# Kernel optimization log

Measured on AMD Instinct MI355X. Metric: run time of the kernel, lower is better.

The kernel has to match this reference:

```python
import jax, jax.numpy as jnp
import numpy as np

N, D, FF, NH = 500000, 128, 256, 4
GRIDS = [0.5, 1.0, 2.0]


def setup_inputs() -> dict:
    key = jax.random.key(0)
    ks = jax.random.split(key, 8)
    h = jax.random.normal(ks[0], (N, D), jnp.float32)
    coords = jax.random.uniform(ks[1], (N, 3), jnp.float32) * 8.0
    c = np.asarray(coords)
    invs, Ms = [], []
    for g in GRIDS:
        vox = np.floor(c / g).astype(np.int64)
        _, inv = np.unique(vox, axis=0, return_inverse=True)
        invs.append(jnp.asarray(inv.reshape(-1).astype(np.int32)))
        Ms.append(int(inv.max()) + 1)
    S = len(GRIDS)
    sc = 0.02
    def rn(k, shape):
        return jax.random.normal(k, shape, jnp.float32) * sc
    params = dict(
        Wqkv=rn(ks[2], (S, 3 * D, D)), bqkv=jnp.zeros((S, 3 * D), jnp.float32),
        Wo=rn(ks[3], (S, D, D)), bo=jnp.zeros((S, D), jnp.float32),
        ln1_s=jnp.ones((S, D), jnp.float32), ln1_b=jnp.zeros((S, D), jnp.float32),
        W1=rn(ks[4], (S, FF, D)), b1=jnp.zeros((S, FF), jnp.float32),
        W2=rn(ks[5], (S, D, FF)), b2=jnp.zeros((S, D), jnp.float32),
        ln2_s=jnp.ones((S, D), jnp.float32), ln2_b=jnp.zeros((S, D), jnp.float32),
        Wf=rn(ks[6], (D, D * (S + 1))), bf=jnp.zeros((D,), jnp.float32),
    )
    return dict(h=h, coords=coords, inv0=invs[0], inv1=invs[1], inv2=invs[2],
                M0=Ms[0], M1=Ms[1], M2=Ms[2], **params)


def _ln(x, s, b):
    m = x.mean(-1, keepdims=True)
    v = ((x - m) ** 2).mean(-1, keepdims=True)
    return (x - m) * jax.lax.rsqrt(v + 1e-5) * s + b


def _forward(h, invs, Ms, Wqkv, bqkv, Wo, bo, ln1_s, ln1_b, W1, b1, W2, b2, ln2_s, ln2_b, Wf, bf):
    dh = D // NH
    feats = [h]
    for i, (inv, M) in enumerate(zip(invs, Ms)):
        # scatter-mean pooling into M voxels (counts clamped >= 1)
        macro = jax.ops.segment_sum(h, inv, num_segments=M)  # [M, D]
        counts = jax.ops.segment_sum(jnp.ones((h.shape[0], 1), h.dtype), inv, num_segments=M)
        macro = macro / jnp.maximum(counts, 1.0)
        # TransformerEncoderLayer (post-norm, relu), batch of 1 -> drop batch dim
        qkv = macro @ Wqkv[i].T + bqkv[i]
        q, k, v = (t.reshape(M, NH, dh) for t in jnp.split(qkv, 3, axis=-1))
        scores = jnp.einsum('mhd,nhd->hmn', q, k) / jnp.sqrt(jnp.float32(dh))
        attn = jax.nn.softmax(scores, axis=-1)
        o = jnp.einsum('hmn,nhd->mhd', attn, v).reshape(M, D) @ Wo[i].T + bo[i]
        x = _ln(macro + o, ln1_s[i], ln1_b[i])
        ffo = jax.nn.relu(x @ W1[i].T + b1[i]) @ W2[i].T + b2[i]
        x = _ln(x + ffo, ln2_s[i], ln2_b[i])
        feats.append(x[inv])  # broadcast gather back to particles [N, D]
    return jnp.concatenate(feats, axis=-1) @ Wf.T + bf


def reference(h, coords, inv0, inv1, inv2, M0, M1, M2, Wqkv, bqkv, Wo, bo, ln1_s, ln1_b, W1, b1, W2, b2, ln2_s, ln2_b, Wf, bf):
    return _forward(h, (inv0, inv1, inv2), (M0, M1, M2), Wqkv, bqkv, Wo, bo,
                    ln1_s, ln1_b, W1, b1, W2, b2, ln2_s, ln2_b, Wf, bf)
```

## Files before the change

kernel.cpp:

```cpp
#include <hip/hip_runtime.h>
#include <hip/hip_bf16.h>

#define MC 4096
#define DD 128
#define NHH 4
#define DH 32
#define FFD 256
#define NS 3
#define NSPLIT 4
#define PLEN 1024

typedef __attribute__((ext_vector_type(8))) short short8_t;
typedef __attribute__((ext_vector_type(4))) float f32x4;

__device__ __forceinline__ int getM(int s, const int* M0, const int* M1, const int* M2) {
    return (s == 0) ? *M0 : (s == 1) ? *M1 : *M2;
}

__device__ __forceinline__ unsigned short f2bf(float f) {
    unsigned int u = __float_as_uint(f);
    u += 0x7FFFu + ((u >> 16) & 1u);
    return (unsigned short)(u >> 16);
}

__device__ __forceinline__ short8_t pack8(float4 a, float4 b) {
    short8_t r;
    r[0] = (short)f2bf(a.x); r[1] = (short)f2bf(a.y);
    r[2] = (short)f2bf(a.z); r[3] = (short)f2bf(a.w);
    r[4] = (short)f2bf(b.x); r[5] = (short)f2bf(b.y);
    r[6] = (short)f2bf(b.z); r[7] = (short)f2bf(b.w);
    return r;
}

__device__ __forceinline__ f32x4 max4(f32x4 a, f32x4 b) {
    f32x4 r;
    r[0] = fmaxf(a[0], b[0]); r[1] = fmaxf(a[1], b[1]);
    r[2] = fmaxf(a[2], b[2]); r[3] = fmaxf(a[3], b[3]);
    return r;
}
__device__ __forceinline__ f32x4 shflx4(f32x4 a, int m) {
    f32x4 r;
    r[0] = __shfl_xor(a[0], m); r[1] = __shfl_xor(a[1], m);
    r[2] = __shfl_xor(a[2], m); r[3] = __shfl_xor(a[3], m);
    return r;
}
__device__ __forceinline__ f32x4 exp4(f32x4 a) {
    f32x4 r;
    r[0] = __expf(a[0]); r[1] = __expf(a[1]);
    r[2] = __expf(a[2]); r[3] = __expf(a[3]);
    return r;
}

__global__ void k_parent(const int* __restrict__ inv0, const int* __restrict__ inv1,
                         const int* __restrict__ inv2,
                         int* __restrict__ parent10, int* __restrict__ parent21,
                         int* __restrict__ cnt, int N)
{
    int n = blockIdx.x * blockDim.x + threadIdx.x;
    if (n >= N) return;
    int i0 = inv0[n];
    parent10[i0] = inv1[n];
    parent21[inv1[n]] = inv2[n];
    atomicAdd(&cnt[i0], 1);
}

__global__ void k_scan(const int* __restrict__ cnt, int* __restrict__ offs)
{
    __shared__ int arr[1024];
    int tid = threadIdx.x;
    int base = tid * 4;
    int c0 = cnt[base], c1 = cnt[base + 1], c2 = cnt[base + 2], c3 = cnt[base + 3];
    int tot = c0 + c1 + c2 + c3;
    arr[tid] = tot;
    __syncthreads();
    for (int off = 1; off < 1024; off <<= 1) {
        int v = (tid >= off) ? arr[tid - off] : 0;
        __syncthreads();
        arr[tid] += v;
        __syncthreads();
    }
    int excl = arr[tid] - tot;
    offs[base] = excl;
    offs[base + 1] = excl + c0;
    offs[base + 2] = excl + c0 + c1;
    offs[base + 3] = excl + c0 + c1 + c2;
}

__global__ void k_place(const int* __restrict__ inv0, const int* __restrict__ offs,
                        int* __restrict__ fill, int* __restrict__ order, int N)
{
    int n = blockIdx.x * blockDim.x + threadIdx.x;
    if (n >= N) return;
    int i0 = inv0[n];
    int pos = offs[i0] + atomicAdd(&fill[i0], 1);
    order[pos] = n;
}

__global__ __launch_bounds__(256) void k_pool(const float* __restrict__ h,
                                              const int* __restrict__ order,
                                              const int* __restrict__ offs,
                                              const int* __restrict__ cnt,
                                              float* __restrict__ sum0, float* __restrict__ cnt0,
                                              const int* __restrict__ M0)
{
    int v = blockIdx.x;
    if (v >= *M0) return;
    int beg = offs[v], len = cnt[v];
    int tid = threadIdx.x;
    int dg = tid & 31;
    int rs = tid >> 5;
    const int* op = order + beg;

    float ax = 0.f, ay = 0.f, az = 0.f, aw = 0.f;
    int j = rs;
    for (; j + 8 < len; j += 16) {
        int r0 = op[j];
        int r1 = op[j + 8];
        float4 a = *(const float4*)(h + (size_t)r0 * DD + dg * 4);
        float4 b = *(const float4*)(h + (size_t)r1 * DD + dg * 4);
        ax += a.x + b.x; ay += a.y + b.y; az += a.z + b.z; aw += a.w + b.w;
    }
    if (j < len) {
        int r0 = op[j];
        float4 a = *(const float4*)(h + (size_t)r0 * DD + dg * 4);
        ax += a.x; ay += a.y; az += a.z; aw += a.w;
    }

    __shared__ __align__(16) float red[8][DD];
    *(float4*)&red[rs][dg * 4] = make_float4(ax, ay, az, aw);
    __syncthreads();
    if (tid < 32) {
        float4 t0 = *(const float4*)&red[0][tid * 4];
        float4 t1 = *(const float4*)&red[1][tid * 4];
        float4 t2 = *(const float4*)&red[2][tid * 4];
        float4 t3 = *(const float4*)&red[3][tid * 4];
        float4 t4 = *(const float4*)&red[4][tid * 4];
        float4 t5 = *(const float4*)&red[5][tid * 4];
        float4 t6 = *(const float4*)&red[6][tid * 4];
        float4 t7 = *(const float4*)&red[7][tid * 4];
        float4 r;
        r.x = ((t0.x + t1.x) + (t2.x + t3.x)) + ((t4.x + t5.x) + (t6.x + t7.x));
        r.y = ((t0.y + t1.y) + (t2.y + t3.y)) + ((t4.y + t5.y) + (t6.y + t7.y));
        r.z = ((t0.z + t1.z) + (t2.z + t3.z)) + ((t4.z + t5.z) + (t6.z + t7.z));
        r.w = ((t0.w + t1.w) + (t2.w + t3.w)) + ((t4.w + t5.w) + (t6.w + t7.w));
        *(float4*)(sum0 + (size_t)v * DD + tid * 4) = r;
        if (tid == 0) cnt0[v] = (float)len;
    }
}

__global__ void k_rollup(const float* __restrict__ sumSrc, const float* __restrict__ cntSrc,
                         const int* __restrict__ parent,
                         float* __restrict__ sumDst, float* __restrict__ cntDst,
                         const int* __restrict__ Msrc, int cap)
{
    int idx = blockIdx.x * blockDim.x + threadIdx.x;
    int v = idx >> 7, d = idx & 127;
    int Ms = *Msrc;
    if (Ms > cap) Ms = cap;
    if (v >= Ms) return;
    int p = parent[v];
    atomicAdd(&sumDst[(size_t)p * DD + d], sumSrc[idx]);
    if (d == 0) atomicAdd(&cntDst[p], cntSrc[v]);
}

__global__ void k_finalize(float* __restrict__ macro, const float* __restrict__ counts,
                           const int* M0, const int* M1, const int* M2)
{
    int idx = blockIdx.x * blockDim.x + threadIdx.x;
    int s = idx / (MC * DD);
    int r = (idx >> 7) & (MC - 1);
    if (r >= getM(s, M0, M1, M2)) return;
    float c = counts[s * MC + r];
    macro[idx] /= fmaxf(c, 1.0f);
}

__global__ void k_b0frag(const float* __restrict__ Wf, unsigned short* __restrict__ b0f)
{
    int idx = blockIdx.x * 256 + threadIdx.x;
    int j = idx & 7, l = (idx >> 3) & 63, kt = (idx >> 9) & 3, nt = idx >> 11;
    int d = nt * 16 + (l & 15);
    int k = kt * 32 + (l >> 4) * 8 + j;
    b0f[idx] = f2bf(Wf[(size_t)d * (4 * DD) + k]);
}

__global__ void k_qkv(const float* __restrict__ macro, const float* __restrict__ Wqkv,
                      const float* __restrict__ bqkv, float* __restrict__ qkv,
                      const int* M0, const int* M1, const int* M2)
{
    int s = blockIdx.y;
    int Ms = getM(s, M0, M1, M2);
    int row0 = blockIdx.x * 8;
    if (row0 >= Ms) return;
    __shared__ __align__(16) float mac[8][DD];
    int tid = threadIdx.x;
    for (int e = tid; e < 8 * DD; e += 256) {
        int r = e >> 7, d = e & 127;
        int row = row0 + r;
        mac[r][d] = (row < Ms) ? macro[(size_t)s * MC * DD + (size_t)row * DD + d] : 0.0f;
    }
    __syncthreads();
    for (int j = tid; j < 3 * DD; j += 256) {
        const float* w = Wqkv + ((size_t)s * 3 * DD + j) * DD;
        float b = bqkv[s * 3 * DD + j];
        float acc[8];
#pragma unroll
        for (int r = 0; r < 8; ++r) acc[r] = b;
        for (int k = 0; k < DD; k += 4) {
            float4 w4 = *(const float4*)(w + k);
#pragma unroll
            for (int r = 0; r < 8; ++r) {
                float4 m4 = *(const float4*)&mac[r][k];
                acc[r] += w4.x * m4.x + w4.y * m4.y + w4.z * m4.z + w4.w * m4.w;
            }
        }
        for (int r = 0; r < 8; ++r) {
            int row = row0 + r;
            if (row < Ms) qkv[((size_t)s * MC + row) * (3 * DD) + j] = acc[r];
        }
    }
}

__global__ __launch_bounds__(256) void k_attn_part(const float* __restrict__ qkv,
                                                   float* __restrict__ part_o,
                                                   float* __restrict__ part_ml,
                                                   const int* M0, const int* M1, const int* M2)
{
    int z = blockIdx.z;
    int s = z / NSPLIT, part = z % NSPLIT;
    int head = blockIdx.y;
    int Ms = getM(s, M0, M1, M2);
    int q0 = blockIdx.x * 64;
    if (q0 >= Ms) return;
    int kstart = part * PLEN;
    if (kstart >= Ms) return;
    int kend = kstart + PLEN; if (kend > Ms) kend = Ms;

    __shared__ __align__(16) unsigned short kf[2][4][64][8];
    __shared__ __align__(16) unsigned short vf[2][2][2][64][8];
    __shared__ __align__(16) unsigned short pf[4][16][80];

    int tid = threadIdx.x;
    int wave = tid >> 6, lane = tid & 63;
    int c = lane & 15, g = lane >> 4;

    const float* base = qkv + (size_t)s * MC * 3 * DD;
    const float* Qb = base + head * DH;
    const float* Kb = base + DD + head * DH;
    const float* Vb = base + 2 * DD + head * DH;

    short8_t qfrag = {0,0,0,0,0,0,0,0};
    {
        int qr = q0 + wave * 16 + c;
        if (qr < Ms) {
            const float* qp = Qb + (size_t)qr * 3 * DD + g * 8;
            qfrag = pack8(*(const float4*)qp, *(const float4*)(qp + 4));
        }
    }

    f32x4 o0 = {0.f, 0.f, 0.f, 0.f}, o1 = {0.f, 0.f, 0.f, 0.f};
    f32x4 mreg = {-1e30f, -1e30f, -1e30f, -1e30f};
    f32x4 lreg = {0.f, 0.f, 0.f, 0.f};
    const float scale = 0.1767766952966369f;

    int sko = tid >> 2, sg = tid & 3;
    int s_nt = sko >> 4;
    int s_l  = (sko & 15) | (sg << 4);
    int s_ks = sko >> 5, s_kk = sko & 31;
    int s_j  = s_kk & 7, s_hi = (s_kk >> 3) & 3;
    int s_vnt = sg >> 1, s_db = (sg & 1) * 8;

    auto STAGE = [&](int buf, int kb) {
        {
            int key = kb + sko;
            short8_t kv = {0,0,0,0,0,0,0,0};
            if (key < kend) {
                const float* kr = Kb + (size_t)key * 3 * DD + sg * 8;
                kv = pack8(*(const float4*)kr, *(const float4*)(kr + 4));
            }
            *(short8_t*)&kf[buf][s_nt][s_l][0] = kv;
        }
        {
            int key = kb + sko;
            float4 a = make_float4(0.f, 0.f, 0.f, 0.f);
            float4 b = make_float4(0.f, 0.f, 0.f, 0.f);
            if (key < kend) {
                const float* vr = Vb + (size_t)key * 3 * DD + sg * 8;
                a = *(const float4*)vr;
                b = *(const float4*)(vr + 4);
            }
            unsigned short* vslot = &vf[buf][s_ks][s_vnt][0][0];
            vslot[((s_db + 0) | (s_hi << 4)) * 8 + s_j] = f2bf(a.x);
            vslot[((s_db + 1) | (s_hi << 4)) * 8 + s_j] = f2bf(a.y);
            vslot[((s_db + 2) | (s_hi << 4)) * 8 + s_j] = f2bf(a.z);
            vslot[((s_db + 3) | (s_hi << 4)) * 8 + s_j] = f2bf(a.w);
            vslot[((s_db + 4) | (s_hi << 4)) * 8 + s_j] = f2bf(b.x);
            vslot[((s_db + 5) | (s_hi << 4)) * 8 + s_j] = f2bf(b.y);
            vslot[((s_db + 6) | (s_hi << 4)) * 8 + s_j] = f2bf(b.z);
            vslot[((s_db + 7) | (s_hi << 4)) * 8 + s_j] = f2bf(b.w);
        }
    };

    STAGE(0, kstart);
    __syncthreads();
    int cur = 0;

    for (int kb = kstart; kb < kend; kb += 64) {
        if (kb + 64 < kend) STAGE(cur ^ 1, kb + 64);

        f32x4 zero = {0.f, 0.f, 0.f, 0.f};
        short8_t kf0 = *(const short8_t*)&kf[cur][0][lane][0];
        short8_t kf1 = *(const short8_t*)&kf[cur][1][lane][0];
        short8_t kf2 = *(const short8_t*)&kf[cur][2][lane][0];
        short8_t kf3 = *(const short8_t*)&kf[cur][3][lane][0];
        f32x4 a0 = __builtin_amdgcn_mfma_f32_16x16x32_bf16(qfrag, kf0, zero, 0, 0, 0);
        f32x4 a1 = __builtin_amdgcn_mfma_f32_16x16x32_bf16(qfrag, kf1, zero, 0, 0, 0);
        f32x4 a2 = __builtin_amdgcn_mfma_f32_16x16x32_bf16(qfrag, kf2, zero, 0, 0, 0);
        f32x4 a3 = __builtin_amdgcn_mfma_f32_16x16x32_bf16(qfrag, kf3, zero, 0, 0, 0);

        f32x4 neg = {-1e30f, -1e30f, -1e30f, -1e30f};
        a0 = (kb +  0 + c < kend) ? a0 * scale : neg;
        a1 = (kb + 16 + c < kend) ? a1 * scale : neg;
        a2 = (kb + 32 + c < kend) ? a2 * scale : neg;
        a3 = (kb + 48 + c < kend) ? a3 * scale : neg;

        f32x4 rmax = max4(max4(a0, a1), max4(a2, a3));
        rmax = max4(rmax, shflx4(rmax, 1));
        rmax = max4(rmax, shflx4(rmax, 2));
        rmax = max4(rmax, shflx4(rmax, 4));
        rmax = max4(rmax, shflx4(rmax, 8));
        f32x4 mnew = max4(mreg, rmax);
        f32x4 alpha = exp4(mreg - mnew);
        mreg = mnew;
        lreg = lreg * alpha;
        o0 = o0 * alpha;
        o1 = o1 * alpha;

        a0 = exp4(a0 - mnew);
        a1 = exp4(a1 - mnew);
        a2 = exp4(a2 - mnew);
        a3 = exp4(a3 - mnew);
        f32x4 rsum = (a0 + a1) + (a2 + a3);
        rsum = rsum + shflx4(rsum, 1);
        rsum = rsum + shflx4(rsum, 2);
        rsum = rsum + shflx4(rsum, 4);
        rsum = rsum + shflx4(rsum, 8);
        lreg = lreg + rsum;

        {
            unsigned short* prow = &pf[wave][0][0];
            int rb = g * 4;
            prow[(rb + 0) * 80 +  0 + c] = f2bf(a0[0]);
            prow[(rb + 1) * 80 +  0 + c] = f2bf(a0[1]);
            prow[(rb + 2) * 80 +  0 + c] = f2bf(a0[2]);
            prow[(rb + 3) * 80 +  0 + c] = f2bf(a0[3]);
            prow[(rb + 0) * 80 + 16 + c] = f2bf(a1[0]);
            prow[(rb + 1) * 80 + 16 + c] = f2bf(a1[1]);
            prow[(rb + 2) * 80 + 16 + c] = f2bf(a1[2]);
            prow[(rb + 3) * 80 + 16 + c] = f2bf(a1[3]);
            prow[(rb + 0) * 80 + 32 + c] = f2bf(a2[0]);
            prow[(rb + 1) * 80 + 32 + c] = f2bf(a2[1]);
            prow[(rb + 2) * 80 + 32 + c] = f2bf(a2[2]);
            prow[(rb + 3) * 80 + 32 + c] = f2bf(a2[3]);
            prow[(rb + 0) * 80 + 48 + c] = f2bf(a3[0]);
            prow[(rb + 1) * 80 + 48 + c] = f2bf(a3[1]);
            prow[(rb + 2) * 80 + 48 + c] = f2bf(a3[2]);
            prow[(rb + 3) * 80 + 48 + c] = f2bf(a3[3]);
        }

        {
            short8_t p0 = *(const short8_t*)&pf[wave][c][ 0 + g * 8];
            short8_t v00 = *(const short8_t*)&vf[cur][0][0][lane][0];
            short8_t v01 = *(const short8_t*)&vf[cur][0][1][lane][0];
            o0 = __builtin_amdgcn_mfma_f32_16x16x32_bf16(p0, v00, o0, 0, 0, 0);
            o1 = __builtin_amdgcn_mfma_f32_16x16x32_bf16(p0, v01, o1, 0, 0, 0);
            short8_t p1 = *(const short8_t*)&pf[wave][c][32 + g * 8];
            short8_t v10 = *(const short8_t*)&vf[cur][1][0][lane][0];
            short8_t v11 = *(const short8_t*)&vf[cur][1][1][lane][0];
            o0 = __builtin_amdgcn_mfma_f32_16x16x32_bf16(p1, v10, o0, 0, 0, 0);
            o1 = __builtin_amdgcn_mfma_f32_16x16x32_bf16(p1, v11, o1, 0, 0, 0);
        }

        __syncthreads();
        cur ^= 1;
    }

    int rec = ((s * NHH + head) * 64 + blockIdx.x) * NSPLIT + part;
    float* po = part_o + (size_t)rec * 2048;
    int qb = wave * 16 + g * 4;
    po[(qb + 0) * 32 + c] = o0[0];
    po[(qb + 1) * 32 + c] = o0[1];
    po[(qb + 2) * 32 + c] = o0[2];
    po[(qb + 3) * 32 + c] = o0[3];
    po[(qb + 0) * 32 + 16 + c] = o1[0];
    po[(qb + 1) * 32 + 16 + c] = o1[1];
    po[(qb + 2) * 32 + 16 + c] = o1[2];
    po[(qb + 3) * 32 + 16 + c] = o1[3];
    if (c == 0) {
        part_ml[rec * 128 + qb + 0] = mreg[0];
        part_ml[rec * 128 + qb + 1] = mreg[1];
        part_ml[rec * 128 + qb + 2] = mreg[2];
        part_ml[rec * 128 + qb + 3] = mreg[3];
        part_ml[rec * 128 + 64 + qb + 0] = lreg[0];
        part_ml[rec * 128 + 64 + qb + 1] = lreg[1];
        part_ml[rec * 128 + 64 + qb + 2] = lreg[2];
        part_ml[rec * 128 + 64 + qb + 3] = lreg[3];
    }
}

__global__ void k_attn_comb(const float* __restrict__ part_o, const float* __restrict__ part_ml,
                            float* __restrict__ attno,
                            const int* M0, const int* M1, const int* M2)
{
    int s = blockIdx.z, head = blockIdx.y;
    int Ms = getM(s, M0, M1, M2);
    int q0 = blockIdx.x * 64;
    if (q0 >= Ms) return;
    int tid = threadIdx.x;
    int qi = tid >> 2, sub = tid & 3;
    int nparts = (Ms + PLEN - 1) / PLEN;
    if (nparts > NSPLIT) nparts = NSPLIT;
    int recbase = ((s * NHH + head) * 64 + blockIdx.x) * NSPLIT;

    float m = -1e30f;
    for (int p = 0; p < nparts; ++p)
        m = fmaxf(m, part_ml[(recbase + p) * 128 + qi]);
    float L = 0.f;
    float4 A0 = {0,0,0,0}, A1 = {0,0,0,0};
    for (int p = 0; p < nparts; ++p) {
        float mp = part_ml[(recbase + p) * 128 + qi];
        float lp = part_ml[(recbase + p) * 128 + 64 + qi];
        float w = __expf(mp - m);
        L += lp * w;
        const float* po = part_o + (size_t)(recbase + p) * 2048;
        float4 a = *(const float4*)(po + qi * 32 + sub * 4);
        float4 b = *(const float4*)(po + qi * 32 + (sub + 4) * 4);
        A0.x += a.x * w; A0.y += a.y * w; A0.z += a.z * w; A0.w += a.w * w;
        A1.x += b.x * w; A1.y += b.y * w; A1.z += b.z * w; A1.w += b.w * w;
    }
    if (q0 + qi < Ms) {
        float inv = 1.0f / fmaxf(L, 1e-30f);
        size_t orow = ((size_t)s * MC + q0 + qi) * DD + head * DH;
        float4 r0 = make_float4(A0.x * inv, A0.y * inv, A0.z * inv, A0.w * inv);
        float4 r1 = make_float4(A1.x * inv, A1.y * inv, A1.z * inv, A1.w * inv);
        *(float4*)(attno + orow + sub * 4) = r0;
        *(float4*)(attno + orow + (sub + 4) * 4) = r1;
    }
}

__global__ __launch_bounds__(256) void k_layer(const float* __restrict__ macro,
                                               const float* __restrict__ attno,
                                               const float* __restrict__ Wo, const float* __restrict__ bo,
                                               const float* __restrict__ ln1s, const float* __restrict__ ln1b,
                                               const float* __restrict__ W1, const float* __restrict__ b1,
                                               const float* __restrict__ W2, const float* __restrict__ b2,
                                               const float* __restrict__ ln2s, const float* __restrict__ ln2b,
                                               const float* __restrict__ Wf,
                                               float* __restrict__ y,
                                               const int* M0, const int* M1, const int* M2)
{
    int s = blockIdx.y;
    int Ms = getM(s, M0, M1, M2);
    int row0 = blockIdx.x * 8;
    if (row0 >= Ms) return;
    __shared__ __align__(16) float os8[8][DD];
    __shared__ __align__(16) float xr8[8][DD];
    __shared__ __align__(16) float ts8[8][FFD];
    __shared__ float mv[8][2];
    int tid = threadIdx.x;
    int rr = tid >> 5, tt = tid & 31;

    {
        int row = row0 + rr;
        float4 v = make_float4(0.f, 0.f, 0.f, 0.f);
        if (row < Ms) v = *(const float4*)(attno + ((size_t)s * MC + row) * DD + tt * 4);
        *(float4*)&os8[rr][tt * 4] = v;
    }
    __syncthreads();

    float acc[8];

    if (tid < DD) {
        const float* w = Wo + ((size_t)s * DD + tid) * DD;
        float b = bo[s * DD + tid];
#pragma unroll
        for (int r = 0; r < 8; ++r) acc[r] = b;
        for (int k = 0; k < DD; k += 4) {
            float4 w4 = *(const float4*)(w + k);
#pragma unroll
            for (int r = 0; r < 8; ++r) {
                float4 m4 = *(const float4*)&os8[r][k];
                acc[r] += w4.x * m4.x + w4.y * m4.y + w4.z * m4.z + w4.w * m4.w;
            }
        }
#pragma unroll
        for (int r = 0; r < 8; ++r) {
            int row = row0 + r;
            float res = (row < Ms) ? macro[((size_t)s * MC + row) * DD + tid] : 0.f;
            xr8[r][tid] = acc[r] + res;
        }
    }
    __syncthreads();

    {
        float4 v = *(const float4*)&xr8[rr][tt * 4];
        float su = v.x + v.y + v.z + v.w;
        float sq = v.x * v.x + v.y * v.y + v.z * v.z + v.w * v.w;
        for (int off = 16; off >= 1; off >>= 1) { su += __shfl_xor(su, off); sq += __shfl_xor(sq, off); }
        if (tt == 0) { mv[rr][0] = su; mv[rr][1] = sq; }
    }
    __syncthreads();
    {
        float mean = mv[rr][0] * (1.0f / DD);
        float var = fmaxf(mv[rr][1] * (1.0f / DD) - mean * mean, 0.0f);
        float rstd = rsqrtf(var + 1e-5f);
        float4 v = *(const float4*)&xr8[rr][tt * 4];
        float4 gs = *(const float4*)(ln1s + s * DD + tt * 4);
        float4 gb = *(const float4*)(ln1b + s * DD + tt * 4);
        float4 o;
        o.x = (v.x - mean) * rstd * gs.x + gb.x;
        o.y = (v.y - mean) * rstd * gs.y + gb.y;
        o.z = (v.z - mean) * rstd * gs.z + gb.z;
        o.w = (v.w - mean) * rstd * gs.w + gb.w;
        *(float4*)&xr8[rr][tt * 4] = o;
    }
    __syncthreads();

    {
        const float* w = W1 + ((size_t)s * FFD + tid) * DD;
        float b = b1[s * FFD + tid];
#pragma unroll
        for (int r = 0; r < 8; ++r) acc[r] = b;
        for (int k = 0; k < DD; k += 4) {
            float4 w4 = *(const float4*)(w + k);
#pragma unroll
            for (int r = 0; r < 8; ++r) {
                float4 m4 = *(const float4*)&xr8[r][k];
                acc[r] += w4.x * m4.x + w4.y * m4.y + w4.z * m4.z + w4.w * m4.w;
            }
        }
#pragma unroll
        for (int r = 0; r < 8; ++r) ts8[r][tid] = fmaxf(acc[r], 0.0f);
    }
    __syncthreads();

    if (tid < DD) {
        const float* w = W2 + ((size_t)s * DD + tid) * FFD;
        float b = b2[s * DD + tid];
#pragma unroll
        for (int r = 0; r < 8; ++r) acc[r] = b;
        for (int k = 0; k < FFD; k += 4) {
            float4 w4 = *(const float4*)(w + k);
#pragma unroll
            for (int r = 0; r < 8; ++r) {
                float4 m4 = *(const float4*)&ts8[r][k];
                acc[r] += w4.x * m4.x + w4.y * m4.y + w4.z * m4.z + w4.w * m4.w;
            }
        }
#pragma unroll
        for (int r = 0; r < 8; ++r) os8[r][tid] = acc[r] + xr8[r][tid];
    }
    __syncthreads();

    {
        float4 v = *(const float4*)&os8[rr][tt * 4];
        float su = v.x + v.y + v.z + v.w;
        float sq = v.x * v.x + v.y * v.y + v.z * v.z + v.w * v.w;
        for (int off = 16; off >= 1; off >>= 1) { su += __shfl_xor(su, off); sq += __shfl_xor(sq, off); }
        if (tt == 0) { mv[rr][0] = su; mv[rr][1] = sq; }
    }
    __syncthreads();
    {
        float mean = mv[rr][0] * (1.0f / DD);
        float var = fmaxf(mv[rr][1] * (1.0f / DD) - mean * mean, 0.0f);
        float rstd = rsqrtf(var + 1e-5f);
        float4 v = *(const float4*)&os8[rr][tt * 4];
        float4 gs = *(const float4*)(ln2s + s * DD + tt * 4);
        float4 gb = *(const float4*)(ln2b + s * DD + tt * 4);
        float4 o;
        o.x = (v.x - mean) * rstd * gs.x + gb.x;
        o.y = (v.y - mean) * rstd * gs.y + gb.y;
        o.z = (v.z - mean) * rstd * gs.z + gb.z;
        o.w = (v.w - mean) * rstd * gs.w + gb.w;
        *(float4*)&os8[rr][tt * 4] = o;
    }
    __syncthreads();

    if (tid < DD) {
        const float* w = Wf + (size_t)tid * (4 * DD) + (s + 1) * DD;
#pragma unroll
        for (int r = 0; r < 8; ++r) acc[r] = 0.f;
        for (int k = 0; k < DD; k += 4) {
            float4 w4 = *(const float4*)(w + k);
#pragma unroll
            for (int r = 0; r < 8; ++r) {
                float4 m4 = *(const float4*)&os8[r][k];
                acc[r] += w4.x * m4.x + w4.y * m4.y + w4.z * m4.z + w4.w * m4.w;
            }
        }
#pragma unroll
        for (int r = 0; r < 8; ++r) {
            int row = row0 + r;
            if (row < Ms) y[((size_t)s * MC + row) * DD + tid] = acc[r];
        }
    }
}

__global__ void k_ycomb(const float* __restrict__ y, const int* __restrict__ parent10,
                        const int* __restrict__ parent21, const float* __restrict__ bf,
                        float* __restrict__ yc, const int* __restrict__ M0)
{
    int idx = blockIdx.x * 256 + threadIdx.x;
    int v = idx >> 7, d = idx & 127;
    if (v >= *M0) return;
    int p1 = parent10[v];
    int p2 = parent21[p1];
    yc[idx] = y[(size_t)v * DD + d] + y[((size_t)MC + p1) * DD + d]
            + y[((size_t)2 * MC + p2) * DD + d] + bf[d];
}

__global__ __launch_bounds__(256) void k_final(const float* __restrict__ h,
                                               const unsigned short* __restrict__ b0f,
                                               const float* __restrict__ yc,
                                               const int* __restrict__ inv0,
                                               float* __restrict__ out, int N)
{
    int tid = threadIdx.x;
    int wave = tid >> 6, lane = tid & 63;
    int c = lane & 15, g = lane >> 4;

    int ntasks = (N + 15) >> 4;
    int pair = blockIdx.x * 4 + wave;
    int taskA = pair * 2;
    if (taskA >= ntasks) return;
    int taskB = taskA + 1;

    int pA = taskA * 16 + c;
    int pB = taskB * 16 + c;
    bool okA = (pA < N);
    bool okB = (taskB < ntasks) && (pB < N);

    short8_t hA0 = {0,0,0,0,0,0,0,0}, hA1 = hA0, hA2 = hA0, hA3 = hA0;
    short8_t hB0 = hA0, hB1 = hA0, hB2 = hA0, hB3 = hA0;
    int iA = 0, iB = 0;
    if (okA) {
        const float* hr = h + (size_t)pA * DD + g * 8;
        hA0 = pack8(*(const float4*)(hr +  0), *(const float4*)(hr +  4));
        hA1 = pack8(*(const float4*)(hr + 32), *(const float4*)(hr + 36));
        hA2 = pack8(*(const float4*)(hr + 64), *(const float4*)(hr + 68));
        hA3 = pack8(*(const float4*)(hr + 96), *(const float4*)(hr + 100));
        iA = inv0[pA];
    }
    if (okB) {
        const float* hr = h + (size_t)pB * DD + g * 8;
        hB0 = pack8(*(const float4*)(hr +  0), *(const float4*)(hr +  4));
        hB1 = pack8(*(const float4*)(hr + 32), *(const float4*)(hr + 36));
        hB2 = pack8(*(const float4*)(hr + 64), *(const float4*)(hr + 68));
        hB3 = pack8(*(const float4*)(hr + 96), *(const float4*)(hr + 100));
        iB = inv0[pB];
    }
    const float* ycA = yc + (size_t)iA * DD;
    const float* ycB = yc + (size_t)iB * DD;

#pragma unroll
    for (int ntp = 0; ntp < 4; ++ntp) {
        int nt0 = ntp * 2, nt1 = ntp * 2 + 1;
        f32x4 aA0 = {0.f, 0.f, 0.f, 0.f}, aA1 = {0.f, 0.f, 0.f, 0.f};
        f32x4 aB0 = {0.f, 0.f, 0.f, 0.f}, aB1 = {0.f, 0.f, 0.f, 0.f};
        {
            short8_t w00 = *(const short8_t*)(b0f + (size_t)((nt0 * 4 + 0) * 64 + lane) * 8);
            aA0 = __builtin_amdgcn_mfma_f32_16x16x32_bf16(w00, hA0, aA0, 0, 0, 0);
            aB0 = __builtin_amdgcn_mfma_f32_16x16x32_bf16(w00, hB0, aB0, 0, 0, 0);
            short8_t w10 = *(const short8_t*)(b0f + (size_t)((nt1 * 4 + 0) * 64 + lane) * 8);
            aA1 = __builtin_amdgcn_mfma_f32_16x16x32_bf16(w10, hA0, aA1, 0, 0, 0);
            aB1 = __builtin_amdgcn_mfma_f32_16x16x32_bf16(w10, hB0, aB1, 0, 0, 0);
            short8_t w01 = *(const short8_t*)(b0f + (size_t)((nt0 * 4 + 1) * 64 + lane) * 8);
            aA0 = __builtin_amdgcn_mfma_f32_16x16x32_bf16(w01, hA1, aA0, 0, 0, 0);
            aB0 = __builtin_amdgcn_mfma_f32_16x16x32_bf16(w01, hB1, aB0, 0, 0, 0);
            short8_t w11 = *(const short8_t*)(b0f + (size_t)((nt1 * 4 + 1) * 64 + lane) * 8);
            aA1 = __builtin_amdgcn_mfma_f32_16x16x32_bf16(w11, hA1, aA1, 0, 0, 0);
            aB1 = __builtin_amdgcn_mfma_f32_16x16x32_bf16(w11, hB1, aB1, 0, 0, 0);
            short8_t w02 = *(const short8_t*)(b0f + (size_t)((nt0 * 4 + 2) * 64 + lane) * 8);
            aA0 = __builtin_amdgcn_mfma_f32_16x16x32_bf16(w02, hA2, aA0, 0, 0, 0);
            aB0 = __builtin_amdgcn_mfma_f32_16x16x32_bf16(w02, hB2, aB0, 0, 0, 0);
            short8_t w12 = *(const short8_t*)(b0f + (size_t)((nt1 * 4 + 2) * 64 + lane) * 8);
            aA1 = __builtin_amdgcn_mfma_f32_16x16x32_bf16(w12, hA2, aA1, 0, 0, 0);
            aB1 = __builtin_amdgcn_mfma_f32_16x16x32_bf16(w12, hB2, aB1, 0, 0, 0);
            short8_t w03 = *(const short8_t*)(b0f + (size_t)((nt0 * 4 + 3) * 64 + lane) * 8);
            aA0 = __builtin_amdgcn_mfma_f32_16x16x32_bf16(w03, hA3, aA0, 0, 0, 0);
            aB0 = __builtin_amdgcn_mfma_f32_16x16x32_bf16(w03, hB3, aB0, 0, 0, 0);
            short8_t w13 = *(const short8_t*)(b0f + (size_t)((nt1 * 4 + 3) * 64 + lane) * 8);
            aA1 = __builtin_amdgcn_mfma_f32_16x16x32_bf16(w13, hA3, aA1, 0, 0, 0);
            aB1 = __builtin_amdgcn_mfma_f32_16x16x32_bf16(w13, hB3, aB1, 0, 0, 0);
        }
        int d0 = nt0 * 16 + g * 4;
        int d1 = d0 + 16;
        if (okA) {
            float4 g0 = *(const float4*)(ycA + d0);
            float4 g1 = *(const float4*)(ycA + d1);
            float4 r0, r1;
            r0.x = aA0[0] + g0.x; r0.y = aA0[1] + g0.y; r0.z = aA0[2] + g0.z; r0.w = aA0[3] + g0.w;
            r1.x = aA1[0] + g1.x; r1.y = aA1[1] + g1.y; r1.z = aA1[2] + g1.z; r1.w = aA1[3] + g1.w;
            *(float4*)(out + (size_t)pA * DD + d0) = r0;
            *(float4*)(out + (size_t)pA * DD + d1) = r1;
        }
        if (okB) {
            float4 g0 = *(const float4*)(ycB + d0);
            float4 g1 = *(const float4*)(ycB + d1);
            float4 r0, r1;
            r0.x = aB0[0] + g0.x; r0.y = aB0[1] + g0.y; r0.z = aB0[2] + g0.z; r0.w = aB0[3] + g0.w;
            r1.x = aB1[0] + g1.x; r1.y = aB1[1] + g1.y; r1.z = aB1[2] + g1.z; r1.w = aB1[3] + g1.w;
            *(float4*)(out + (size_t)pB * DD + d0) = r0;
            *(float4*)(out + (size_t)pB * DD + d1) = r1;
        }
    }
}

extern "C" void kernel_launch(void* const* d_in, const int* in_sizes, int n_in,
                              void* d_out, int out_size, void* d_ws, size_t ws_size,
                              hipStream_t stream) {
    (void)n_in; (void)out_size; (void)ws_size;
    const float* h   = (const float*)d_in[0];
    const int* inv0  = (const int*)d_in[2];
    const int* inv1  = (const int*)d_in[3];
    const int* inv2  = (const int*)d_in[4];
    const int* M0    = (const int*)d_in[5];
    const int* M1    = (const int*)d_in[6];
    const int* M2    = (const int*)d_in[7];
    const float* Wqkv = (const float*)d_in[8];
    const float* bqkv = (const float*)d_in[9];
    const float* Wo   = (const float*)d_in[10];
    const float* bo   = (const float*)d_in[11];
    const float* ln1s = (const float*)d_in[12];
    const float* ln1b = (const float*)d_in[13];
    const float* W1   = (const float*)d_in[14];
    const float* b1   = (const float*)d_in[15];
    const float* W2   = (const float*)d_in[16];
    const float* b2   = (const float*)d_in[17];
    const float* ln2s = (const float*)d_in[18];
    const float* ln2b = (const float*)d_in[19];
    const float* Wf   = (const float*)d_in[20];
    const float* bf   = (const float*)d_in[21];
    int N = in_sizes[0] / DD;

    float* ws      = (float*)d_ws;
    float* macro   = ws;
    float* counts  = macro + (size_t)NS * MC * DD;
    float* qkvb    = counts + (size_t)NS * MC;
    float* attno   = qkvb + (size_t)NS * MC * 3 * DD;
    float* yb      = attno + (size_t)NS * MC * DD;
    float* b0f_f   = yb + (size_t)NS * MC * DD;
    unsigned short* b0f = (unsigned short*)b0f_f;
    float* part_o  = b0f_f + (size_t)DD * DD;
    float* part_ml = part_o + (size_t)NS * NHH * 64 * NSPLIT * 2048;
    float* ycb     = part_ml + (size_t)NS * NHH * 64 * NSPLIT * 128;
    int* ip        = (int*)(ycb + (size_t)MC * DD);
    int* parent10  = ip;
    int* parent21  = parent10 + MC;
    int* cnt_i     = parent21 + 512;
    int* fill      = cnt_i + MC;
    int* offs      = fill + MC;
    int* order     = offs + MC;

    float* sum0 = macro;
    float* sum1 = macro + (size_t)1 * MC * DD;
    float* sum2 = macro + (size_t)2 * MC * DD;
    float* cnt0 = counts;
    float* cnt1 = counts + MC;
    float* cnt2 = counts + 2 * MC;

    hipMemsetAsync(macro, 0, ((size_t)NS * MC * DD + NS * MC) * sizeof(float), stream);
    hipMemsetAsync(cnt_i, 0, (size_t)2 * MC * sizeof(int), stream);

    int nb = (N + 255) / 256;
    k_parent<<<nb, 256, 0, stream>>>(inv0, inv1, inv2, parent10, parent21, cnt_i, N);
    k_scan<<<1, 1024, 0, stream>>>(cnt_i, offs);
    k_place<<<nb, 256, 0, stream>>>(inv0, offs, fill, order, N);
    k_pool<<<MC, 256, 0, stream>>>(h, order, offs, cnt_i, sum0, cnt0, M0);
    k_rollup<<<(MC * DD) / 256, 256, 0, stream>>>(sum0, cnt0, parent10, sum1, cnt1, M0, MC);
    k_rollup<<<(512 * DD) / 256, 256, 0, stream>>>(sum1, cnt1, parent21, sum2, cnt2, M1, 512);
    k_finalize<<<(NS * MC * DD) / 256, 256, 0, stream>>>(macro, counts, M0, M1, M2);
    k_b0frag<<<64, 256, 0, stream>>>(Wf, b0f);
    k_qkv<<<dim3(MC / 8, NS), 256, 0, stream>>>(macro, Wqkv, bqkv, qkvb, M0, M1, M2);
    k_attn_part<<<dim3(MC / 64, NHH, NS * NSPLIT), 256, 0, stream>>>(qkvb, part_o, part_ml, M0, M1, M2);
    k_attn_comb<<<dim3(MC / 64, NHH, NS), 256, 0, stream>>>(part_o, part_ml, attno, M0, M1, M2);
    k_layer<<<dim3(MC / 8, NS), 256, 0, stream>>>(macro, attno, Wo, bo, ln1s, ln1b,
                                                  W1, b1, W2, b2, ln2s, ln2b, Wf, yb, M0, M1, M2);
    k_ycomb<<<(MC * DD) / 256, 256, 0, stream>>>(yb, parent10, parent21, bf, ycb, M0);
    int ntasks = (N + 15) >> 4;
    int npairs = (ntasks + 1) / 2;
    k_final<<<(npairs + 3) / 4, 256, 0, stream>>>(h, b0f, ycb, inv0, (float*)d_out, N);
}
```

Measured before the change: 460.4 us.

## Merge rollup passes, fold b0frag into finalize, drop ycomb by gathering three levels

Replaces the two sequential rollup launches with one kernel that adds each level-0 voxel sum directly into both its level-1 and level-2 parents. The Wf bf16 fragment conversion is folded into the finalize launch. The ycomb kernel and its buffer are removed; the final kernel instead reads inv1/inv2 per particle and gathers the three per-scale y rows plus bias itself. This cuts launches, but the final kernel now issues three times as many gather loads per particle over N=500k points, plus extra index loads.

```diff
diff --git a/kernel.cpp b/kernel.cpp
--- a/kernel.cpp
+++ b/kernel.cpp
@@ -148,39 +148,45 @@
     }
 }
 
-__global__ void k_rollup(const float* __restrict__ sumSrc, const float* __restrict__ cntSrc,
-                         const int* __restrict__ parent,
-                         float* __restrict__ sumDst, float* __restrict__ cntDst,
-                         const int* __restrict__ Msrc, int cap)
+__global__ void k_rollup_both(const float* __restrict__ sum0, const float* __restrict__ cnt0,
+                              const int* __restrict__ parent10, const int* __restrict__ parent21,
+                              float* __restrict__ sum1, float* __restrict__ cnt1,
+                              float* __restrict__ sum2, float* __restrict__ cnt2,
+                              const int* __restrict__ M0)
 {
     int idx = blockIdx.x * blockDim.x + threadIdx.x;
     int v = idx >> 7, d = idx & 127;
-    int Ms = *Msrc;
-    if (Ms > cap) Ms = cap;
-    if (v >= Ms) return;
-    int p = parent[v];
-    atomicAdd(&sumDst[(size_t)p * DD + d], sumSrc[idx]);
-    if (d == 0) atomicAdd(&cntDst[p], cntSrc[v]);
+    if (v >= *M0) return;
+    int p1 = parent10[v];
+    int p2 = parent21[p1];
+    float val = sum0[idx];
+    atomicAdd(&sum1[(size_t)p1 * DD + d], val);
+    atomicAdd(&sum2[(size_t)p2 * DD + d], val);
+    if (d == 0) {
+        float c = cnt0[v];
+        atomicAdd(&cnt1[p1], c);
+        atomicAdd(&cnt2[p2], c);
+    }
 }
 
 __global__ void k_finalize(float* __restrict__ macro, const float* __restrict__ counts,
+                           const float* __restrict__ Wf, unsigned short* __restrict__ b0f,
                            const int* M0, const int* M1, const int* M2)
 {
     int idx = blockIdx.x * blockDim.x + threadIdx.x;
-    int s = idx / (MC * DD);
-    int r = (idx >> 7) & (MC - 1);
-    if (r >= getM(s, M0, M1, M2)) return;
-    float c = counts[s * MC + r];
-    macro[idx] /= fmaxf(c, 1.0f);
-}
-
-__global__ void k_b0frag(const float* __restrict__ Wf, unsigned short* __restrict__ b0f)
-{
-    int idx = blockIdx.x * 256 + threadIdx.x;
-    int j = idx & 7, l = (idx >> 3) & 63, kt = (idx >> 9) & 3, nt = idx >> 11;
-    int d = nt * 16 + (l & 15);
-    int k = kt * 32 + (l >> 4) * 8 + j;
-    b0f[idx] = f2bf(Wf[(size_t)d * (4 * DD) + k]);
+    if (idx < NS * MC * DD) {
+        int s = idx / (MC * DD);
+        int r = (idx >> 7) & (MC - 1);
+        if (r >= getM(s, M0, M1, M2)) return;
+        float c = counts[s * MC + r];
+        macro[idx] /= fmaxf(c, 1.0f);
+    } else {
+        int e = idx - NS * MC * DD;
+        int j = e & 7, l = (e >> 3) & 63, kt = (e >> 9) & 3, nt = e >> 11;
+        int d = nt * 16 + (l & 15);
+        int k = kt * 32 + (l >> 4) * 8 + j;
+        b0f[e] = f2bf(Wf[(size_t)d * (4 * DD) + k]);
+    }
 }
 
 __global__ void k_qkv(const float* __restrict__ macro, const float* __restrict__ Wqkv,
@@ -605,28 +611,21 @@
     }
 }
 
-__global__ void k_ycomb(const float* __restrict__ y, const int* __restrict__ parent10,
-                        const int* __restrict__ parent21, const float* __restrict__ bf,
-                        float* __restrict__ yc, const int* __restrict__ M0)
-{
-    int idx = blockIdx.x * 256 + threadIdx.x;
-    int v = idx >> 7, d = idx & 127;
-    if (v >= *M0) return;
-    int p1 = parent10[v];
-    int p2 = parent21[p1];
-    yc[idx] = y[(size_t)v * DD + d] + y[((size_t)MC + p1) * DD + d]
-            + y[((size_t)2 * MC + p2) * DD + d] + bf[d];
-}
-
 __global__ __launch_bounds__(256) void k_final(const float* __restrict__ h,
                                                const unsigned short* __restrict__ b0f,
-                                               const float* __restrict__ yc,
+                                               const float* __restrict__ y,
                                                const int* __restrict__ inv0,
+                                               const int* __restrict__ inv1,
+                                               const int* __restrict__ inv2,
+                                               const float* __restrict__ bf,
                                                float* __restrict__ out, int N)
 {
     int tid = threadIdx.x;
     int wave = tid >> 6, lane = tid & 63;
     int c = lane & 15, g = lane >> 4;
+    const float* y0 = y;
+    const float* y1 = y + (size_t)MC * DD;
+    const float* y2 = y + (size_t)2 * MC * DD;
 
     int ntasks = (N + 15) >> 4;
     int pair = blockIdx.x * 4 + wave;
@@ -641,14 +640,14 @@
 
     short8_t hA0 = {0,0,0,0,0,0,0,0}, hA1 = hA0, hA2 = hA0, hA3 = hA0;
     short8_t hB0 = hA0, hB1 = hA0, hB2 = hA0, hB3 = hA0;
-    int iA = 0, iB = 0;
+    int iA0 = 0, iA1 = 0, iA2 = 0, iB0 = 0, iB1 = 0, iB2 = 0;
     if (okA) {
         const float* hr = h + (size_t)pA * DD + g * 8;
         hA0 = pack8(*(const float4*)(hr +  0), *(const float4*)(hr +  4));
         hA1 = pack8(*(const float4*)(hr + 32), *(const float4*)(hr + 36));
         hA2 = pack8(*(const float4*)(hr + 64), *(const float4*)(hr + 68));
         hA3 = pack8(*(const float4*)(hr + 96), *(const float4*)(hr + 100));
-        iA = inv0[pA];
+        iA0 = inv0[pA]; iA1 = inv1[pA]; iA2 = inv2[pA];
     }
     if (okB) {
         const float* hr = h + (size_t)pB * DD + g * 8;
@@ -656,10 +655,14 @@
         hB1 = pack8(*(const float4*)(hr + 32), *(const float4*)(hr + 36));
         hB2 = pack8(*(const float4*)(hr + 64), *(const float4*)(hr + 68));
         hB3 = pack8(*(const float4*)(hr + 96), *(const float4*)(hr + 100));
-        iB = inv0[pB];
-    }
-    const float* ycA = yc + (size_t)iA * DD;
-    const float* ycB = yc + (size_t)iB * DD;
+        iB0 = inv0[pB]; iB1 = inv1[pB]; iB2 = inv2[pB];
+    }
+    const float* yA0 = y0 + (size_t)iA0 * DD;
+    const float* yA1 = y1 + (size_t)iA1 * DD;
+    const float* yA2 = y2 + (size_t)iA2 * DD;
+    const float* yB0 = y0 + (size_t)iB0 * DD;
+    const float* yB1 = y1 + (size_t)iB1 * DD;
+    const float* yB2 = y2 + (size_t)iB2 * DD;
 
 #pragma unroll
     for (int ntp = 0; ntp < 4; ++ntp) {
@@ -695,20 +698,44 @@
         int d0 = nt0 * 16 + g * 4;
         int d1 = d0 + 16;
         if (okA) {
-            float4 g0 = *(const float4*)(ycA + d0);
-            float4 g1 = *(const float4*)(ycA + d1);
+            float4 gA00 = *(const float4*)(yA0 + d0);
+            float4 gA10 = *(const float4*)(yA1 + d0);
+            float4 gA20 = *(const float4*)(yA2 + d0);
+            float4 b40 = *(const float4*)(bf + d0);
+            float4 gA01 = *(const float4*)(yA0 + d1);
+            float4 gA11 = *(const float4*)(yA1 + d1);
+            float4 gA21 = *(const float4*)(yA2 + d1);
+            float4 b41 = *(const float4*)(bf + d1);
             float4 r0, r1;
-            r0.x = aA0[0] + g0.x; r0.y = aA0[1] + g0.y; r0.z = aA0[2] + g0.z; r0.w = aA0[3] + g0.w;
-            r1.x = aA1[0] + g1.x; r1.y = aA1[1] + g1.y; r1.z = aA1[2] + g1.z; r1.w = aA1[3] + g1.w;
+            r0.x = aA0[0] + gA00.x + gA10.x + gA20.x + b40.x;
+            r0.y = aA0[1] + gA00.y + gA10.y + gA20.y + b40.y;
+            r0.z = aA0[2] + gA00.z + gA10.z + gA20.z + b40.z;
+            r0.w = aA0[3] + gA00.w + gA10.w + gA20.w + b40.w;
+            r1.x = aA1[0] + gA01.x + gA11.x + gA21.x + b41.x;
+            r1.y = aA1[1] + gA01.y + gA11.y + gA21.y + b41.y;
+            r1.z = aA1[2] + gA01.z + gA11.z + gA21.z + b41.z;
+            r1.w = aA1[3] + gA01.w + gA11.w + gA21.w + b41.w;
             *(float4*)(out + (size_t)pA * DD + d0) = r0;
             *(float4*)(out + (size_t)pA * DD + d1) = r1;
         }
         if (okB) {
-            float4 g0 = *(const float4*)(ycB + d0);
-            float4 g1 = *(const float4*)(ycB + d1);
+            float4 gB00 = *(const float4*)(yB0 + d0);
+            float4 gB10 = *(const float4*)(yB1 + d0);
+            float4 gB20 = *(const float4*)(yB2 + d0);
+            float4 b40 = *(const float4*)(bf + d0);
+            float4 gB01 = *(const float4*)(yB0 + d1);
+            float4 gB11 = *(const float4*)(yB1 + d1);
+            float4 gB21 = *(const float4*)(yB2 + d1);
+            float4 b41 = *(const float4*)(bf + d1);
             float4 r0, r1;
-            r0.x = aB0[0] + g0.x; r0.y = aB0[1] + g0.y; r0.z = aB0[2] + g0.z; r0.w = aB0[3] + g0.w;
-            r1.x = aB1[0] + g1.x; r1.y = aB1[1] + g1.y; r1.z = aB1[2] + g1.z; r1.w = aB1[3] + g1.w;
+            r0.x = aB0[0] + gB00.x + gB10.x + gB20.x + b40.x;
+            r0.y = aB0[1] + gB00.y + gB10.y + gB20.y + b40.y;
+            r0.z = aB0[2] + gB00.z + gB10.z + gB20.z + b40.z;
+            r0.w = aB0[3] + gB00.w + gB10.w + gB20.w + b40.w;
+            r1.x = aB1[0] + gB01.x + gB11.x + gB21.x + b41.x;
+            r1.y = aB1[1] + gB01.y + gB11.y + gB21.y + b41.y;
+            r1.z = aB1[2] + gB01.z + gB11.z + gB21.z + b41.z;
+            r1.w = aB1[3] + gB01.w + gB11.w + gB21.w + b41.w;
             *(float4*)(out + (size_t)pB * DD + d0) = r0;
             *(float4*)(out + (size_t)pB * DD + d1) = r1;
         }
@@ -752,8 +779,7 @@
     unsigned short* b0f = (unsigned short*)b0f_f;
     float* part_o  = b0f_f + (size_t)DD * DD;
     float* part_ml = part_o + (size_t)NS * NHH * 64 * NSPLIT * 2048;
-    float* ycb     = part_ml + (size_t)NS * NHH * 64 * NSPLIT * 128;
-    int* ip        = (int*)(ycb + (size_t)MC * DD);
+    int* ip        = (int*)(part_ml + (size_t)NS * NHH * 64 * NSPLIT * 128);
     int* parent10  = ip;
     int* parent21  = parent10 + MC;
     int* cnt_i     = parent21 + 512;
@@ -776,17 +802,15 @@
     k_scan<<<1, 1024, 0, stream>>>(cnt_i, offs);
     k_place<<<nb, 256, 0, stream>>>(inv0, offs, fill, order, N);
     k_pool<<<MC, 256, 0, stream>>>(h, order, offs, cnt_i, sum0, cnt0, M0);
-    k_rollup<<<(MC * DD) / 256, 256, 0, stream>>>(sum0, cnt0, parent10, sum1, cnt1, M0, MC);
-    k_rollup<<<(512 * DD) / 256, 256, 0, stream>>>(sum1, cnt1, parent21, sum2, cnt2, M1, 512);
-    k_finalize<<<(NS * MC * DD) / 256, 256, 0, stream>>>(macro, counts, M0, M1, M2);
-    k_b0frag<<<64, 256, 0, stream>>>(Wf, b0f);
+    k_rollup_both<<<(MC * DD) / 256, 256, 0, stream>>>(sum0, cnt0, parent10, parent21,
+                                                       sum1, cnt1, sum2, cnt2, M0);
+    k_finalize<<<(NS * MC * DD + DD * DD) / 256, 256, 0, stream>>>(macro, counts, Wf, b0f, M0, M1, M2);
     k_qkv<<<dim3(MC / 8, NS), 256, 0, stream>>>(macro, Wqkv, bqkv, qkvb, M0, M1, M2);
     k_attn_part<<<dim3(MC / 64, NHH, NS * NSPLIT), 256, 0, stream>>>(qkvb, part_o, part_ml, M0, M1, M2);
     k_attn_comb<<<dim3(MC / 64, NHH, NS), 256, 0, stream>>>(part_o, part_ml, attno, M0, M1, M2);
     k_layer<<<dim3(MC / 8, NS), 256, 0, stream>>>(macro, attno, Wo, bo, ln1s, ln1b,
                                                   W1, b1, W2, b2, ln2s, ln2b, Wf, yb, M0, M1, M2);
-    k_ycomb<<<(MC * DD) / 256, 256, 0, stream>>>(yb, parent10, parent21, bf, ycb, M0);
     int ntasks = (N + 15) >> 4;
     int npairs = (ntasks + 1) / 2;
-    k_final<<<(npairs + 3) / 4, 256, 0, stream>>>(h, b0f, ycb, inv0, (float*)d_out, N);
-}
+    k_final<<<(npairs + 3) / 4, 256, 0, stream>>>(h, b0f, yb, inv0, inv1, inv2, bf, (float*)d_out, N);
+}
```

Result: slower. 523.5 us (+13.7%).
